# Performance work log

Measured on AMD Instinct MI355X. Metric: run time of the kernel, lower is better.

The kernel has to match this reference:

```python
import jax, jax.numpy as jnp
import numpy as np

N_NODES = 50000
N_EDGES = 800000
NODE_DIM = 64
MSG_DIM = 64
EDGE_DIM = 4
ROUNDS = 2


def setup_inputs() -> dict:
    key = jax.random.key(0)
    ks = jax.random.split(key, 10)
    in_dim = 2 * NODE_DIM + EDGE_DIM  # cat([src hv, dst hv, he])
    return {
        "hv": jax.random.normal(ks[0], (N_NODES, NODE_DIM), dtype=jnp.float32),
        "he": jax.random.uniform(ks[1], (N_EDGES, EDGE_DIM), dtype=jnp.float32),
        "W_msg": jax.random.normal(ks[2], (ROUNDS, in_dim, MSG_DIM), dtype=jnp.float32) * 0.05,
        "b_msg": jax.random.normal(ks[3], (ROUNDS, MSG_DIM), dtype=jnp.float32) * 0.05,
        "W_ih": jax.random.normal(ks[4], (ROUNDS, MSG_DIM, 3 * NODE_DIM), dtype=jnp.float32) * 0.05,
        "W_hh": jax.random.normal(ks[5], (ROUNDS, NODE_DIM, 3 * NODE_DIM), dtype=jnp.float32) * 0.05,
        "b_ih": jax.random.normal(ks[6], (ROUNDS, 3 * NODE_DIM), dtype=jnp.float32) * 0.05,
        "b_hh": jax.random.normal(ks[7], (ROUNDS, 3 * NODE_DIM), dtype=jnp.float32) * 0.05,
        "src": jax.random.randint(ks[8], (N_EDGES,), 0, N_NODES, dtype=jnp.int64)
        if jax.config.jax_enable_x64 else jax.random.randint(ks[8], (N_EDGES,), 0, N_NODES).astype(jnp.int32),
        "dst": jax.random.randint(ks[9], (N_EDGES,), 0, N_NODES).astype(jnp.int32),
    }


def gru_cell(a, h, W_ih, W_hh, b_ih, b_hh):
    # torch.nn.GRUCell math; gate order (r, z, n) along the 3H axis
    gi = a @ W_ih + b_ih   # [N, 3H]
    gh = h @ W_hh + b_hh   # [N, 3H]
    i_r, i_z, i_n = jnp.split(gi, 3, axis=1)
    h_r, h_z, h_n = jnp.split(gh, 3, axis=1)
    r = jax.nn.sigmoid(i_r + h_r)
    z = jax.nn.sigmoid(i_z + h_z)
    n = jnp.tanh(i_n + r * h_n)
    return (1.0 - z) * n + z * h


def reference(hv, he, W_msg, b_msg, W_ih, W_hh, b_ih, b_hh, src, dst):
    # GraphProp.forward: per-round gather -> message MLP -> scatter-sum -> GRU update
    N = hv.shape[0]
    src = src.astype(jnp.int32)
    dst = dst.astype(jnp.int32)
    rounds = W_msg.shape[0]
    for t in range(rounds):
        # dgmg_msg: m = cat([src hv, dst hv, he])  [E, 2*D+E_dim]
        m_in = jnp.concatenate([hv[src], hv[dst], he], axis=1)
        msg = m_in @ W_msg[t] + b_msg[t]  # message_funcs[t] (Linear + Identity)
        # dgmg_reduce: sum of inbound messages per destination node
        a = jax.ops.segment_sum(msg, dst, num_segments=N)  # [N, MSG_DIM]
        hv = gru_cell(a, hv, W_ih[t], W_hh[t], b_ih[t], b_hh[t])
    return hv
```

## Files before the change

### kernel.cpp

```cpp
#include <hip/hip_runtime.h>

#define N_NODES 50000
#define N_EDGES 800000
#define D 64
#define EDIM 4
#define IN_DIM 132
#define H3 192


__global__ void k_count(const int* __restrict__ dst, int* __restrict__ deg) {
    int e = blockIdx.x * blockDim.x + threadIdx.x;
    if (e < N_EDGES) atomicAdd(&deg[dst[e]], 1);
}

__global__ __launch_bounds__(256) void k_scan1(const int* __restrict__ deg,
                                               int* __restrict__ offsets,
                                               int* __restrict__ bsum) {
    __shared__ int sm[256];
    int tid = threadIdx.x;
    int i = blockIdx.x * 256 + tid;
    int x = (i < N_NODES) ? deg[i] : 0;
    sm[tid] = x;
    __syncthreads();
    for (int s = 1; s < 256; s <<= 1) {
        int v = (tid >= s) ? sm[tid - s] : 0;
        __syncthreads();
        sm[tid] += v;
        __syncthreads();
    }
    if (i < N_NODES) offsets[i] = sm[tid] - x;
    if (tid == 255) bsum[blockIdx.x] = sm[255];
}

__global__ __launch_bounds__(256) void k_scan2(const int* __restrict__ bsum,
                                               int* __restrict__ boff, int nblk) {
    __shared__ int sm[256];
    int tid = threadIdx.x;
    int x = (tid < nblk) ? bsum[tid] : 0;
    sm[tid] = x;
    __syncthreads();
    for (int s = 1; s < 256; s <<= 1) {
        int v = (tid >= s) ? sm[tid - s] : 0;
        __syncthreads();
        sm[tid] += v;
        __syncthreads();
    }
    if (tid < nblk) boff[tid] = sm[tid] - x;
}

__global__ __launch_bounds__(256) void k_scan3(int* __restrict__ offsets,
                                               const int* __restrict__ boff) {
    int i = blockIdx.x * 256 + threadIdx.x;
    if (i < N_NODES) offsets[i] += boff[blockIdx.x];
}

__global__ void k_fill(const int* __restrict__ src, const int* __restrict__ dst,
                       const int* __restrict__ offsets, int* __restrict__ cursor,
                       int* __restrict__ csr_src, int* __restrict__ csr_eid) {
    int e = blockIdx.x * blockDim.x + threadIdx.x;
    if (e < N_EDGES) {
        int d = dst[e];
        int pos = offsets[d] + atomicAdd(&cursor[d], 1);
        csr_src[pos] = src[e];
        csr_eid[pos] = e;
    }
}


template <int ROUND>
__global__ __launch_bounds__(256) void k_reduce(const float* __restrict__ hv,
                                                const float* __restrict__ he,
                                                const int* __restrict__ csr_src,
                                                const int* __restrict__ csr_eid,
                                                const int* __restrict__ offsets,
                                                const int* __restrict__ deg,
                                                float* __restrict__ S,
                                                float* __restrict__ Hsum) {
    int wave = (blockIdx.x * blockDim.x + threadIdx.x) >> 6;
    if (wave >= N_NODES) return;
    int lane = threadIdx.x & 63;
    int g = lane >> 4;
    int c = lane & 15;
    const int off = offsets[wave];
    const int cnt = deg[wave];
    float4 acc = make_float4(0.f, 0.f, 0.f, 0.f);
    float4 hacc = make_float4(0.f, 0.f, 0.f, 0.f);
    for (int e = g; e < cnt; e += 4) {
        int sn = csr_src[off + e];
        float4 v = ((const float4*)(hv + (size_t)sn * D))[c];
        acc.x += v.x; acc.y += v.y; acc.z += v.z; acc.w += v.w;
        if (ROUND == 0 && c == 0) {
            int eid = csr_eid[off + e];
            float4 h = *(const float4*)(he + (size_t)eid * EDIM);
            hacc.x += h.x; hacc.y += h.y; hacc.z += h.z; hacc.w += h.w;
        }
    }
    acc.x += __shfl_xor(acc.x, 16); acc.y += __shfl_xor(acc.y, 16);
    acc.z += __shfl_xor(acc.z, 16); acc.w += __shfl_xor(acc.w, 16);
    acc.x += __shfl_xor(acc.x, 32); acc.y += __shfl_xor(acc.y, 32);
    acc.z += __shfl_xor(acc.z, 32); acc.w += __shfl_xor(acc.w, 32);
    if (ROUND == 0) {
        hacc.x += __shfl_xor(hacc.x, 16); hacc.y += __shfl_xor(hacc.y, 16);
        hacc.z += __shfl_xor(hacc.z, 16); hacc.w += __shfl_xor(hacc.w, 16);
        hacc.x += __shfl_xor(hacc.x, 32); hacc.y += __shfl_xor(hacc.y, 32);
        hacc.z += __shfl_xor(hacc.z, 32); hacc.w += __shfl_xor(hacc.w, 32);
    }
    if (g == 0) ((float4*)(S + (size_t)wave * D))[c] = acc;
    if (ROUND == 0 && lane == 0) *(float4*)(Hsum + (size_t)wave * EDIM) = hacc;
}


__global__ __launch_bounds__(512) void k_node(const float* __restrict__ hv_in,
                                              const float* __restrict__ S,
                                              const float* __restrict__ Hsum,
                                              const int* __restrict__ deg,
                                              const float* __restrict__ W_msg,
                                              const float* __restrict__ b_msg,
                                              const float* __restrict__ W_ih,
                                              const float* __restrict__ W_hh,
                                              const float* __restrict__ b_ih,
                                              const float* __restrict__ b_hh,
                                              float* __restrict__ hv_out, int t) {
    __shared__ float XT[IN_DIM * D];

    const int tid = threadIdx.x;
    const int n_base = blockIdx.x * D;

    {
        int nl = tid >> 3;
        int c = tid & 7;
        int n = n_base + nl;
        if (n >= N_NODES) n = N_NODES - 1;
        const float4* Sp = (const float4*)(S + (size_t)n * D);
        const float4* Hp = (const float4*)(hv_in + (size_t)n * D);
        float4 s0 = Sp[c * 2], s1 = Sp[c * 2 + 1];
        float4 h0 = Hp[c * 2], h1 = Hp[c * 2 + 1];
        int k0 = c * 8;
        XT[(k0 + 0) * D + nl] = s0.x; XT[(k0 + 1) * D + nl] = s0.y;
        XT[(k0 + 2) * D + nl] = s0.z; XT[(k0 + 3) * D + nl] = s0.w;
        XT[(k0 + 4) * D + nl] = s1.x; XT[(k0 + 5) * D + nl] = s1.y;
        XT[(k0 + 6) * D + nl] = s1.z; XT[(k0 + 7) * D + nl] = s1.w;
        XT[(64 + k0 + 0) * D + nl] = h0.x; XT[(64 + k0 + 1) * D + nl] = h0.y;
        XT[(64 + k0 + 2) * D + nl] = h0.z; XT[(64 + k0 + 3) * D + nl] = h0.w;
        XT[(64 + k0 + 4) * D + nl] = h1.x; XT[(64 + k0 + 5) * D + nl] = h1.y;
        XT[(64 + k0 + 6) * D + nl] = h1.z; XT[(64 + k0 + 7) * D + nl] = h1.w;
        if (c == 0) {
            float4 hs = *(const float4*)(Hsum + (size_t)n * EDIM);
            XT[128 * D + nl] = hs.x; XT[129 * D + nl] = hs.y;
            XT[130 * D + nl] = hs.z; XT[131 * D + nl] = hs.w;
        }
    }
    __syncthreads();

    const int lane = tid & 63;
    const int w = __builtin_amdgcn_readfirstlane(tid) >> 6;
    const int jb = w * 8;
    const int n = n_base + lane;
    const bool nvalid = (n < N_NODES);
    const int nc = nvalid ? n : N_NODES - 1;
    const float degf = (float)deg[nc];

    const float* __restrict__ Wm = W_msg + (size_t)t * IN_DIM * D;

    float acc1[8], acc2[8];
#pragma unroll
    for (int i = 0; i < 8; ++i) { acc1[i] = 0.f; acc2[i] = 0.f; }

#pragma unroll 4
    for (int k = 0; k < 64; ++k) {
        float aS = XT[k * D + lane];
        float aH = XT[(64 + k) * D + lane];
        const float* wr1 = Wm + k * D + jb;
        const float* wr2 = Wm + (64 + k) * D + jb;
#pragma unroll
        for (int i = 0; i < 8; ++i) {
            acc1[i] = fmaf(aS, wr1[i], acc1[i]);
            acc2[i] = fmaf(aH, wr2[i], acc2[i]);
        }
    }
#pragma unroll
    for (int q = 0; q < 4; ++q) {
        float aQ = XT[(128 + q) * D + lane];
        const float* wr = Wm + (128 + q) * D + jb;
#pragma unroll
        for (int i = 0; i < 8; ++i) acc1[i] = fmaf(aQ, wr[i], acc1[i]);
    }

    const float* bmp = b_msg + (size_t)t * D + jb;
    float av[8];
#pragma unroll
    for (int i = 0; i < 8; ++i) av[i] = acc1[i] + degf * (acc2[i] + bmp[i]);

    __syncthreads();
#pragma unroll
    for (int i = 0; i < 8; ++i) XT[(jb + i) * D + lane] = av[i];
    __syncthreads();

    const float* __restrict__ Wi = W_ih + (size_t)t * D * H3;
    const float* __restrict__ Wh = W_hh + (size_t)t * D * H3;
    const float* bi = b_ih + (size_t)t * H3;
    const float* bh = b_hh + (size_t)t * H3;

    float aR[8], aZ[8], aN[8], aHN[8];
#pragma unroll
    for (int i = 0; i < 8; ++i) {
        aR[i] = bi[jb + i] + bh[jb + i];
        aZ[i] = bi[64 + jb + i] + bh[64 + jb + i];
        aN[i] = bi[128 + jb + i];
        aHN[i] = bh[128 + jb + i];
    }

#pragma unroll 4
    for (int k = 0; k < 64; ++k) {
        float Aa = XT[k * D + lane];
        const float* wr = Wi + k * H3;
#pragma unroll
        for (int i = 0; i < 8; ++i) {
            aR[i] = fmaf(Aa, wr[jb + i], aR[i]);
            aZ[i] = fmaf(Aa, wr[64 + jb + i], aZ[i]);
            aN[i] = fmaf(Aa, wr[128 + jb + i], aN[i]);
        }
    }
#pragma unroll 4
    for (int k = 0; k < 64; ++k) {
        float Ah = XT[(64 + k) * D + lane];
        const float* wr = Wh + k * H3;
#pragma unroll
        for (int i = 0; i < 8; ++i) {
            aR[i] = fmaf(Ah, wr[jb + i], aR[i]);
            aZ[i] = fmaf(Ah, wr[64 + jb + i], aZ[i]);
            aHN[i] = fmaf(Ah, wr[128 + jb + i], aHN[i]);
        }
    }

    float o[8];
#pragma unroll
    for (int i = 0; i < 8; ++i) {
        float r = 1.f / (1.f + __expf(-aR[i]));
        float z = 1.f / (1.f + __expf(-aZ[i]));
        float nin = aN[i] + r * aHN[i];
        float nn = 2.f / (1.f + __expf(-2.f * nin)) - 1.f;
        float hold = XT[(64 + jb + i) * D + lane];
        o[i] = (1.f - z) * nn + z * hold;
    }
    if (nvalid) {
        float4* op = (float4*)(hv_out + (size_t)n * D + jb);
        op[0] = make_float4(o[0], o[1], o[2], o[3]);
        op[1] = make_float4(o[4], o[5], o[6], o[7]);
    }
}


extern "C" void kernel_launch(void* const* d_in, const int* in_sizes, int n_in,
                              void* d_out, int out_size, void* d_ws, size_t ws_size,
                              hipStream_t stream) {
    const float* hv = (const float*)d_in[0];
    const float* he = (const float*)d_in[1];
    const float* W_msg = (const float*)d_in[2];
    const float* b_msg = (const float*)d_in[3];
    const float* W_ih = (const float*)d_in[4];
    const float* W_hh = (const float*)d_in[5];
    const float* b_ih = (const float*)d_in[6];
    const float* b_hh = (const float*)d_in[7];
    const int* src = (const int*)d_in[8];
    const int* dst = (const int*)d_in[9];
    float* out = (float*)d_out;

    char* p = (char*)d_ws;
    int* deg = (int*)p;        p += (size_t)N_NODES * sizeof(int);
    int* cursor = (int*)p;     p += (size_t)N_NODES * sizeof(int);
    int* offsets = (int*)p;    p += (size_t)N_NODES * sizeof(int);
    int* bsum = (int*)p;       p += 256 * sizeof(int);
    int* boff = (int*)p;       p += 256 * sizeof(int);
    int* csr_src = (int*)p;    p += (size_t)N_EDGES * sizeof(int);
    float* Hsum = (float*)p;   p += (size_t)N_NODES * EDIM * sizeof(float);
    float* S = (float*)p;      p += (size_t)N_NODES * D * sizeof(float);
    float* hv_buf = (float*)p; p += (size_t)N_NODES * D * sizeof(float);
    int* csr_eid = (int*)hv_buf;

    const int NBLK = (N_NODES + 255) / 256;

    hipMemsetAsync(deg, 0, N_NODES * sizeof(int), stream);
    hipMemsetAsync(cursor, 0, N_NODES * sizeof(int), stream);

    k_count<<<(N_EDGES + 255) / 256, 256, 0, stream>>>(dst, deg);
    k_scan1<<<NBLK, 256, 0, stream>>>(deg, offsets, bsum);
    k_scan2<<<1, 256, 0, stream>>>(bsum, boff, NBLK);
    k_scan3<<<NBLK, 256, 0, stream>>>(offsets, boff);
    k_fill<<<(N_EDGES + 255) / 256, 256, 0, stream>>>(src, dst, offsets, cursor, csr_src, csr_eid);

    const int RBLK = (N_NODES * 64 + 255) / 256;
    const int GBLK = (N_NODES + 63) / 64;

    k_reduce<0><<<RBLK, 256, 0, stream>>>(hv, he, csr_src, csr_eid, offsets, deg, S, Hsum);
    k_node<<<GBLK, 512, 0, stream>>>(hv, S, Hsum, deg, W_msg, b_msg, W_ih, W_hh, b_ih, b_hh, hv_buf, 0);

    k_reduce<1><<<RBLK, 256, 0, stream>>>(hv_buf, he, csr_src, csr_eid, offsets, deg, S, Hsum);
    k_node<<<GBLK, 512, 0, stream>>>(hv_buf, S, Hsum, deg, W_msg, b_msg, W_ih, W_hh, b_ih, b_hh, out, 1);
}
```

Measured before the change: 432.7 us.

## Fuse CSR neighbor gather-reduce into the node GRU kernel per round

Merges the per-destination gather-sum kernel into the node update kernel. Each block now aggregates neighbor features for its own 64 nodes straight into shared memory, so the S intermediate no longer makes a round trip through global memory and two launches per round go away. The shared tile stride is padded to 65 to reduce bank conflicts, and csr_eid gets its own workspace slot instead of aliasing hv_buf. The trade-off is fewer independent waves for the latency-bound gather (782 blocks of 512 threads, with each wave looping over 8 nodes) and a larger LDS footprint, which may lower occupancy.

```diff
diff --git a/kernel.cpp b/kernel.cpp
--- a/kernel.cpp
+++ b/kernel.cpp
@@ -6,6 +6,7 @@
 #define EDIM 4
 #define IN_DIM 132
 #define H3 192
+#define XS 65
 
 
 __global__ void k_count(const int* __restrict__ dst, int* __restrict__ deg) {
@@ -68,91 +69,93 @@
 
 
 template <int ROUND>
-__global__ __launch_bounds__(256) void k_reduce(const float* __restrict__ hv,
-                                                const float* __restrict__ he,
-                                                const int* __restrict__ csr_src,
-                                                const int* __restrict__ csr_eid,
-                                                const int* __restrict__ offsets,
-                                                const int* __restrict__ deg,
-                                                float* __restrict__ S,
-                                                float* __restrict__ Hsum) {
-    int wave = (blockIdx.x * blockDim.x + threadIdx.x) >> 6;
-    if (wave >= N_NODES) return;
-    int lane = threadIdx.x & 63;
-    int g = lane >> 4;
-    int c = lane & 15;
-    const int off = offsets[wave];
-    const int cnt = deg[wave];
-    float4 acc = make_float4(0.f, 0.f, 0.f, 0.f);
-    float4 hacc = make_float4(0.f, 0.f, 0.f, 0.f);
-    for (int e = g; e < cnt; e += 4) {
-        int sn = csr_src[off + e];
-        float4 v = ((const float4*)(hv + (size_t)sn * D))[c];
-        acc.x += v.x; acc.y += v.y; acc.z += v.z; acc.w += v.w;
-        if (ROUND == 0 && c == 0) {
-            int eid = csr_eid[off + e];
-            float4 h = *(const float4*)(he + (size_t)eid * EDIM);
-            hacc.x += h.x; hacc.y += h.y; hacc.z += h.z; hacc.w += h.w;
-        }
-    }
-    acc.x += __shfl_xor(acc.x, 16); acc.y += __shfl_xor(acc.y, 16);
-    acc.z += __shfl_xor(acc.z, 16); acc.w += __shfl_xor(acc.w, 16);
-    acc.x += __shfl_xor(acc.x, 32); acc.y += __shfl_xor(acc.y, 32);
-    acc.z += __shfl_xor(acc.z, 32); acc.w += __shfl_xor(acc.w, 32);
-    if (ROUND == 0) {
-        hacc.x += __shfl_xor(hacc.x, 16); hacc.y += __shfl_xor(hacc.y, 16);
-        hacc.z += __shfl_xor(hacc.z, 16); hacc.w += __shfl_xor(hacc.w, 16);
-        hacc.x += __shfl_xor(hacc.x, 32); hacc.y += __shfl_xor(hacc.y, 32);
-        hacc.z += __shfl_xor(hacc.z, 32); hacc.w += __shfl_xor(hacc.w, 32);
-    }
-    if (g == 0) ((float4*)(S + (size_t)wave * D))[c] = acc;
-    if (ROUND == 0 && lane == 0) *(float4*)(Hsum + (size_t)wave * EDIM) = hacc;
-}
-
-
-__global__ __launch_bounds__(512) void k_node(const float* __restrict__ hv_in,
-                                              const float* __restrict__ S,
-                                              const float* __restrict__ Hsum,
-                                              const int* __restrict__ deg,
-                                              const float* __restrict__ W_msg,
-                                              const float* __restrict__ b_msg,
-                                              const float* __restrict__ W_ih,
-                                              const float* __restrict__ W_hh,
-                                              const float* __restrict__ b_ih,
-                                              const float* __restrict__ b_hh,
-                                              float* __restrict__ hv_out, int t) {
-    __shared__ float XT[IN_DIM * D];
+__global__ __launch_bounds__(512) void k_fused(const float* __restrict__ hv_in,
+                                               const float* __restrict__ he,
+                                               const int* __restrict__ csr_src,
+                                               const int* __restrict__ csr_eid,
+                                               const int* __restrict__ offsets,
+                                               const int* __restrict__ deg,
+                                               float* __restrict__ Hsum,
+                                               const float* __restrict__ W_msg,
+                                               const float* __restrict__ b_msg,
+                                               const float* __restrict__ W_ih,
+                                               const float* __restrict__ W_hh,
+                                               const float* __restrict__ b_ih,
+                                               const float* __restrict__ b_hh,
+                                               float* __restrict__ hv_out) {
+    __shared__ float XT[IN_DIM * XS];
 
     const int tid = threadIdx.x;
     const int n_base = blockIdx.x * D;
+    const int lane = tid & 63;
 
     {
         int nl = tid >> 3;
-        int c = tid & 7;
+        int c8 = tid & 7;
         int n = n_base + nl;
         if (n >= N_NODES) n = N_NODES - 1;
-        const float4* Sp = (const float4*)(S + (size_t)n * D);
         const float4* Hp = (const float4*)(hv_in + (size_t)n * D);
-        float4 s0 = Sp[c * 2], s1 = Sp[c * 2 + 1];
-        float4 h0 = Hp[c * 2], h1 = Hp[c * 2 + 1];
-        int k0 = c * 8;
-        XT[(k0 + 0) * D + nl] = s0.x; XT[(k0 + 1) * D + nl] = s0.y;
-        XT[(k0 + 2) * D + nl] = s0.z; XT[(k0 + 3) * D + nl] = s0.w;
-        XT[(k0 + 4) * D + nl] = s1.x; XT[(k0 + 5) * D + nl] = s1.y;
-        XT[(k0 + 6) * D + nl] = s1.z; XT[(k0 + 7) * D + nl] = s1.w;
-        XT[(64 + k0 + 0) * D + nl] = h0.x; XT[(64 + k0 + 1) * D + nl] = h0.y;
-        XT[(64 + k0 + 2) * D + nl] = h0.z; XT[(64 + k0 + 3) * D + nl] = h0.w;
-        XT[(64 + k0 + 4) * D + nl] = h1.x; XT[(64 + k0 + 5) * D + nl] = h1.y;
-        XT[(64 + k0 + 6) * D + nl] = h1.z; XT[(64 + k0 + 7) * D + nl] = h1.w;
-        if (c == 0) {
+        float4 h0 = Hp[c8 * 2], h1 = Hp[c8 * 2 + 1];
+        int k0 = c8 * 8;
+        XT[(64 + k0 + 0) * XS + nl] = h0.x; XT[(64 + k0 + 1) * XS + nl] = h0.y;
+        XT[(64 + k0 + 2) * XS + nl] = h0.z; XT[(64 + k0 + 3) * XS + nl] = h0.w;
+        XT[(64 + k0 + 4) * XS + nl] = h1.x; XT[(64 + k0 + 5) * XS + nl] = h1.y;
+        XT[(64 + k0 + 6) * XS + nl] = h1.z; XT[(64 + k0 + 7) * XS + nl] = h1.w;
+        if (ROUND != 0 && c8 == 0) {
             float4 hs = *(const float4*)(Hsum + (size_t)n * EDIM);
-            XT[128 * D + nl] = hs.x; XT[129 * D + nl] = hs.y;
-            XT[130 * D + nl] = hs.z; XT[131 * D + nl] = hs.w;
-        }
-    }
-    __syncthreads();
-
-    const int lane = tid & 63;
+            XT[128 * XS + nl] = hs.x; XT[129 * XS + nl] = hs.y;
+            XT[130 * XS + nl] = hs.z; XT[131 * XS + nl] = hs.w;
+        }
+    }
+
+    {
+        const int w8 = (tid >> 6) * 8;
+        const int g = lane >> 4;
+        const int c = lane & 15;
+        for (int q = 0; q < 8; ++q) {
+            const int nl = w8 + q;
+            int n = n_base + nl;
+            const bool nv = (n < N_NODES);
+            if (!nv) n = N_NODES - 1;
+            const int off = offsets[n];
+            const int cnt = deg[n];
+            float4 acc = make_float4(0.f, 0.f, 0.f, 0.f);
+            float4 hacc = make_float4(0.f, 0.f, 0.f, 0.f);
+            for (int e = g; e < cnt; e += 4) {
+                int sn = csr_src[off + e];
+                float4 v = ((const float4*)(hv_in + (size_t)sn * D))[c];
+                acc.x += v.x; acc.y += v.y; acc.z += v.z; acc.w += v.w;
+                if (ROUND == 0 && c == 0) {
+                    int eid = csr_eid[off + e];
+                    float4 h = *(const float4*)(he + (size_t)eid * EDIM);
+                    hacc.x += h.x; hacc.y += h.y; hacc.z += h.z; hacc.w += h.w;
+                }
+            }
+            acc.x += __shfl_xor(acc.x, 16); acc.y += __shfl_xor(acc.y, 16);
+            acc.z += __shfl_xor(acc.z, 16); acc.w += __shfl_xor(acc.w, 16);
+            acc.x += __shfl_xor(acc.x, 32); acc.y += __shfl_xor(acc.y, 32);
+            acc.z += __shfl_xor(acc.z, 32); acc.w += __shfl_xor(acc.w, 32);
+            if (g == 0) {
+                XT[(4 * c + 0) * XS + nl] = acc.x;
+                XT[(4 * c + 1) * XS + nl] = acc.y;
+                XT[(4 * c + 2) * XS + nl] = acc.z;
+                XT[(4 * c + 3) * XS + nl] = acc.w;
+            }
+            if (ROUND == 0) {
+                hacc.x += __shfl_xor(hacc.x, 16); hacc.y += __shfl_xor(hacc.y, 16);
+                hacc.z += __shfl_xor(hacc.z, 16); hacc.w += __shfl_xor(hacc.w, 16);
+                hacc.x += __shfl_xor(hacc.x, 32); hacc.y += __shfl_xor(hacc.y, 32);
+                hacc.z += __shfl_xor(hacc.z, 32); hacc.w += __shfl_xor(hacc.w, 32);
+                if (lane == 0) {
+                    XT[128 * XS + nl] = hacc.x; XT[129 * XS + nl] = hacc.y;
+                    XT[130 * XS + nl] = hacc.z; XT[131 * XS + nl] = hacc.w;
+                    if (nv) *(float4*)(Hsum + (size_t)n * EDIM) = hacc;
+                }
+            }
+        }
+    }
+    __syncthreads();
+
     const int w = __builtin_amdgcn_readfirstlane(tid) >> 6;
     const int jb = w * 8;
     const int n = n_base + lane;
@@ -160,7 +163,7 @@
     const int nc = nvalid ? n : N_NODES - 1;
     const float degf = (float)deg[nc];
 
-    const float* __restrict__ Wm = W_msg + (size_t)t * IN_DIM * D;
+    const float* __restrict__ Wm = W_msg + (size_t)ROUND * IN_DIM * D;
 
     float acc1[8], acc2[8];
 #pragma unroll
@@ -168,8 +171,8 @@
 
 #pragma unroll 4
     for (int k = 0; k < 64; ++k) {
-        float aS = XT[k * D + lane];
-        float aH = XT[(64 + k) * D + lane];
+        float aS = XT[k * XS + lane];
+        float aH = XT[(64 + k) * XS + lane];
         const float* wr1 = Wm + k * D + jb;
         const float* wr2 = Wm + (64 + k) * D + jb;
 #pragma unroll
@@ -180,26 +183,26 @@
     }
 #pragma unroll
     for (int q = 0; q < 4; ++q) {
-        float aQ = XT[(128 + q) * D + lane];
+        float aQ = XT[(128 + q) * XS + lane];
         const float* wr = Wm + (128 + q) * D + jb;
 #pragma unroll
         for (int i = 0; i < 8; ++i) acc1[i] = fmaf(aQ, wr[i], acc1[i]);
     }
 
-    const float* bmp = b_msg + (size_t)t * D + jb;
+    const float* bmp = b_msg + (size_t)ROUND * D + jb;
     float av[8];
 #pragma unroll
     for (int i = 0; i < 8; ++i) av[i] = acc1[i] + degf * (acc2[i] + bmp[i]);
 
     __syncthreads();
 #pragma unroll
-    for (int i = 0; i < 8; ++i) XT[(jb + i) * D + lane] = av[i];
-    __syncthreads();
-
-    const float* __restrict__ Wi = W_ih + (size_t)t * D * H3;
-    const float* __restrict__ Wh = W_hh + (size_t)t * D * H3;
-    const float* bi = b_ih + (size_t)t * H3;
-    const float* bh = b_hh + (size_t)t * H3;
+    for (int i = 0; i < 8; ++i) XT[(jb + i) * XS + lane] = av[i];
+    __syncthreads();
+
+    const float* __restrict__ Wi = W_ih + (size_t)ROUND * D * H3;
+    const float* __restrict__ Wh = W_hh + (size_t)ROUND * D * H3;
+    const float* bi = b_ih + (size_t)ROUND * H3;
+    const float* bh = b_hh + (size_t)ROUND * H3;
 
     float aR[8], aZ[8], aN[8], aHN[8];
 #pragma unroll
@@ -212,7 +215,7 @@
 
 #pragma unroll 4
     for (int k = 0; k < 64; ++k) {
-        float Aa = XT[k * D + lane];
+        float Aa = XT[k * XS + lane];
         const float* wr = Wi + k * H3;
 #pragma unroll
         for (int i = 0; i < 8; ++i) {
@@ -223,7 +226,7 @@
     }
 #pragma unroll 4
     for (int k = 0; k < 64; ++k) {
-        float Ah = XT[(64 + k) * D + lane];
+        float Ah = XT[(64 + k) * XS + lane];
         const float* wr = Wh + k * H3;
 #pragma unroll
         for (int i = 0; i < 8; ++i) {
@@ -240,7 +243,7 @@
         float z = 1.f / (1.f + __expf(-aZ[i]));
         float nin = aN[i] + r * aHN[i];
         float nn = 2.f / (1.f + __expf(-2.f * nin)) - 1.f;
-        float hold = XT[(64 + jb + i) * D + lane];
+        float hold = XT[(64 + jb + i) * XS + lane];
         o[i] = (1.f - z) * nn + z * hold;
     }
     if (nvalid) {
@@ -273,10 +276,9 @@
     int* bsum = (int*)p;       p += 256 * sizeof(int);
     int* boff = (int*)p;       p += 256 * sizeof(int);
     int* csr_src = (int*)p;    p += (size_t)N_EDGES * sizeof(int);
+    int* csr_eid = (int*)p;    p += (size_t)N_EDGES * sizeof(int);
     float* Hsum = (float*)p;   p += (size_t)N_NODES * EDIM * sizeof(float);
-    float* S = (float*)p;      p += (size_t)N_NODES * D * sizeof(float);
     float* hv_buf = (float*)p; p += (size_t)N_NODES * D * sizeof(float);
-    int* csr_eid = (int*)hv_buf;
 
     const int NBLK = (N_NODES + 255) / 256;
 
@@ -289,12 +291,11 @@
     k_scan3<<<NBLK, 256, 0, stream>>>(offsets, boff);
     k_fill<<<(N_EDGES + 255) / 256, 256, 0, stream>>>(src, dst, offsets, cursor, csr_src, csr_eid);
 
-    const int RBLK = (N_NODES * 64 + 255) / 256;
     const int GBLK = (N_NODES + 63) / 64;
 
-    k_reduce<0><<<RBLK, 256, 0, stream>>>(hv, he, csr_src, csr_eid, offsets, deg, S, Hsum);
-    k_node<<<GBLK, 512, 0, stream>>>(hv, S, Hsum, deg, W_msg, b_msg, W_ih, W_hh, b_ih, b_hh, hv_buf, 0);
-
-    k_reduce<1><<<RBLK, 256, 0, stream>>>(hv_buf, he, csr_src, csr_eid, offsets, deg, S, Hsum);
-    k_node<<<GBLK, 512, 0, stream>>>(hv_buf, S, Hsum, deg, W_msg, b_msg, W_ih, W_hh, b_ih, b_hh, out, 1);
-}
+    k_fused<0><<<GBLK, 512, 0, stream>>>(hv, he, csr_src, csr_eid, offsets, deg, Hsum,
+                                         W_msg, b_msg, W_ih, W_hh, b_ih, b_hh, hv_buf);
+
+    k_fused<1><<<GBLK, 512, 0, stream>>>(hv_buf, he, csr_src, csr_eid, offsets, deg, Hsum,
+                                         W_msg, b_msg, W_ih, W_hh, b_ih, b_hh, out);
+}
```

Result: slower. 457.8 us (+5.8%).
